# Kernel tuning notes

Hardware: AMD Instinct MI355X
Metric: run time of the kernel (lower is better)

Reference implementation:

```python
import jax, jax.numpy as jnp
import numpy as np
from jax import lax

B, S, PH, N = 4, 512, 4096, 16384
D, G, H, L, FF, GS = 1024, 128, 8, 4, 4096, 32
HD = D // H


def setup_inputs() -> dict:
    key = jax.random.key(0)
    ks = list(jax.random.split(key, 16))
    r = lambda k, sh: jax.random.normal(k, sh, jnp.float32) * 0.02
    return {
        'last_hidden': jax.random.normal(ks[0], (B, S, PH), jnp.float32),
        'current_pointcloud': jax.random.normal(ks[1], (B, N, 3), jnp.float32),
        'fp_w': r(ks[2], (D, PH)), 'fp_b': jnp.zeros((D,), jnp.float32),
        'sp_w': r(ks[3], (G * D, D)), 'sp_b': jnp.zeros((G * D,), jnp.float32),
        'pos_embed': r(ks[4], (1, G, D)),
        'ln1_w': jnp.ones((L, D), jnp.float32), 'ln1_b': jnp.zeros((L, D), jnp.float32),
        'in_w': r(ks[5], (L, 3 * D, D)), 'in_b': jnp.zeros((L, 3 * D), jnp.float32),
        'out_w': r(ks[6], (L, D, D)), 'out_b': jnp.zeros((L, D), jnp.float32),
        'ln2_w': jnp.ones((L, D), jnp.float32), 'ln2_b': jnp.zeros((L, D), jnp.float32),
        'mlp_w1': r(ks[7], (L, FF, D)), 'mlp_b1': jnp.zeros((L, FF), jnp.float32),
        'mlp_w2': r(ks[8], (L, D, FF)), 'mlp_b2': jnp.zeros((L, D), jnp.float32),
        'c1_w': r(ks[9], (D, D)), 'c1_b': jnp.zeros((D,), jnp.float32),
        'bn_g': jnp.ones((D,), jnp.float32), 'bn_beta': jnp.zeros((D,), jnp.float32),
        'bn_m': jnp.zeros((D,), jnp.float32), 'bn_v': jnp.ones((D,), jnp.float32),
        'c2_w': r(ks[10], (3 * GS, D)), 'c2_b': jnp.zeros((3 * GS,), jnp.float32),
    }


def _ln(x, w, b):
    m = jnp.mean(x, -1, keepdims=True)
    v = jnp.mean(jnp.square(x - m), -1, keepdims=True)
    return (x - m) * lax.rsqrt(v + 1e-5) * w + b


def _fps(xyz, num_samples):
    # iterative farthest point sampling; deterministic start index 0
    Bb, Nn, _ = xyz.shape
    dist0 = jnp.full((Bb, Nn), 1e10, xyz.dtype)
    far0 = jnp.zeros((Bb,), jnp.int32)

    def step(carry, _):
        dist, far = carry
        centroid = jnp.take_along_axis(xyz, far[:, None, None], axis=1)  # [B,1,3]
        d = jnp.sum(jnp.square(xyz - centroid), -1)                      # [B,N]
        dist = jnp.minimum(dist, d)
        return (dist, jnp.argmax(dist, -1).astype(jnp.int32)), far

    _, cents = lax.scan(step, (dist0, far0), None, length=num_samples)
    cents = cents.T  # [B, num_samples]
    return jnp.take_along_axis(xyz, cents[:, :, None], axis=1)  # [B,num_samples,3]


def reference(last_hidden, current_pointcloud, fp_w, fp_b, sp_w, sp_b, pos_embed,
              ln1_w, ln1_b, in_w, in_b, out_w, out_b, ln2_w, ln2_b,
              mlp_w1, mlp_b1, mlp_w2, mlp_b2,
              c1_w, c1_b, bn_g, bn_beta, bn_m, bn_v, c2_w, c2_b):
    bsz = last_hidden.shape[0]
    agg = jnp.mean(last_hidden @ fp_w.T + fp_b, axis=1)          # [B,D]
    x = (agg @ sp_w.T + sp_b).reshape(bsz, G, D)                 # [B,G,D]
    centers = _fps(current_pointcloud, G)                        # [B,G,3]
    scale = 1.0 / np.sqrt(HD).astype(np.float32)

    def block(x, p):
        l1w, l1b, iw, ib, ow, ob, l2w, l2b, w1, b1, w2, b2 = p
        xn = _ln(x + pos_embed, l1w, l1b)
        qkv = xn @ iw.T + ib                                     # [B,G,3D]
        q, k, v = jnp.split(qkv, 3, axis=-1)
        hsp = lambda t: t.reshape(bsz, G, H, HD).transpose(0, 2, 1, 3)
        q, k, v = hsp(q), hsp(k), hsp(v)
        a = jax.nn.softmax(jnp.einsum('bhqd,bhkd->bhqk', q, k) * scale, axis=-1)
        o = jnp.einsum('bhqk,bhkd->bhqd', a, v).transpose(0, 2, 1, 3).reshape(bsz, G, D)
        x = x + o @ ow.T + ob
        h = jax.nn.gelu(_ln(x, l2w, l2b) @ w1.T + b1, approximate=False)
        return x + h @ w2.T + b2, None

    x, _ = lax.scan(block, x, (ln1_w, ln1_b, in_w, in_b, out_w, out_b,
                               ln2_w, ln2_b, mlp_w1, mlp_b1, mlp_w2, mlp_b2))

    # future_predictor: 1x1 conv == per-token linear; BN in eval mode
    h = x @ c1_w.T + c1_b
    h = jax.nn.relu((h - bn_m) * lax.rsqrt(bn_v + 1e-5) * bn_g + bn_beta)
    deltas = (h @ c2_w.T + c2_b).reshape(bsz * G, GS, 3)
    pred = deltas + centers.reshape(bsz * G, 1, 3)
    return pred.reshape(bsz, G * GS, 3)
```

## Files before the change

kernel.cpp:

```cpp
#include <hip/hip_runtime.h>
#include <hip/hip_bf16.h>
#include <math.h>


typedef __bf16 bf16x8_t __attribute__((ext_vector_type(8)));
typedef float  f32x4_t  __attribute__((ext_vector_type(4)));

__device__ __forceinline__ float wredsum(float v){
#pragma unroll
  for (int o = 32; o; o >>= 1) v += __shfl_down(v, o, 64);
  return v;
}

__device__ __forceinline__ bf16x8_t pack8(float4 a, float4 b){
  bf16x8_t v;
  v[0]=(__bf16)a.x; v[1]=(__bf16)a.y; v[2]=(__bf16)a.z; v[3]=(__bf16)a.w;
  v[4]=(__bf16)b.x; v[5]=(__bf16)b.y; v[6]=(__bf16)b.z; v[7]=(__bf16)b.w;
  return v;
}

__device__ __forceinline__ void gload16(const void* g, void* l){
  __builtin_amdgcn_global_load_lds((const __attribute__((address_space(1))) unsigned int*)g,
                                   (__attribute__((address_space(3))) unsigned int*)l, 16, 0, 0);
}

__global__ __launch_bounds__(1024) void fused_front(
  const float* __restrict__ pc, float* __restrict__ centers,
  const float* __restrict__ agg, const float* __restrict__ spw,
  const float* __restrict__ spb, float* __restrict__ x,
  const float* __restrict__ inw, const float* __restrict__ outw,
  const float* __restrict__ w1, const float* __restrict__ w2,
  __bf16* __restrict__ wbf)
{
  const int bid = blockIdx.x;
  const int tid = threadIdx.x;
  if (bid < 4){
    const int b = bid;
    const int lane = tid & 63;
    const float* base = pc + (size_t)b * 16384 * 3;
    float px[16], py[16], pz[16], dist[16];
    {
      union { float4 v4[12]; float f[48]; } u;
      const float4* src = (const float4*)(base + tid * 48);
#pragma unroll
      for (int q = 0; q < 12; ++q) u.v4[q] = src[q];
#pragma unroll
      for (int j = 0; j < 16; ++j){
        px[j] = u.f[j*3]; py[j] = u.f[j*3+1]; pz[j] = u.f[j*3+2];
        dist[j] = 1e10f;
      }
    }
    __shared__ unsigned long long keyslot[128];
    for (int i = tid; i < 128; i += 1024) keyslot[i] = 0ULL;
    __syncthreads();
    float cx = base[0], cy = base[1], cz = base[2];
    for (int t = 0; t < 128; ++t){
      if (tid == 0){
        centers[(b*128+t)*3+0] = cx;
        centers[(b*128+t)*3+1] = cy;
        centers[(b*128+t)*3+2] = cz;
      }
      if (t == 127) break;
      float bmax = -1.0f; int bidx = 0;
#pragma unroll
      for (int j = 0; j < 16; ++j){
        float dx = __fsub_rn(px[j], cx);
        float dy = __fsub_rn(py[j], cy);
        float dz = __fsub_rn(pz[j], cz);
        float d  = __fadd_rn(__fadd_rn(__fmul_rn(dx,dx), __fmul_rn(dy,dy)), __fmul_rn(dz,dz));
        float nd = fminf(dist[j], d);
        dist[j] = nd;
        if (nd > bmax){ bmax = nd; bidx = tid*16 + j; }
      }
      unsigned long long key = ((unsigned long long)__float_as_uint(bmax) << 32)
                             | (unsigned long long)(0xFFFFFFFFu - (unsigned)bidx);
#pragma unroll
      for (int o = 32; o; o >>= 1){
        unsigned long long ok = __shfl_down(key, o, 64);
        if (ok > key) key = ok;
      }
      if (lane == 0) atomicMax(&keyslot[t], key);
      __syncthreads();
      const unsigned long long gk = keyslot[t];
      const unsigned gidx = 0xFFFFFFFFu - (unsigned)(gk & 0xFFFFFFFFu);
      const float* cp = base + (size_t)gidx*3;
      cx = cp[0]; cy = cp[1]; cz = cp[2];
    }
  } else if (bid < 1028){
    __shared__ float ag[4096];
    for (int i = tid; i < 4096; i += 1024) ag[i] = agg[i];
    __syncthreads();
    const int wv = tid >> 6, lane = tid & 63;
    const int rbase = ((bid - 4)*16 + wv)*8;
    for (int rr = 0; rr < 8; ++rr){
      const int row = rbase + rr;
      const float* wp = spw + (size_t)row*1024 + lane*4;
      const float4 w0 = *(const float4*)(wp      );
      const float4 wq1 = *(const float4*)(wp + 256);
      const float4 wq2 = *(const float4*)(wp + 512);
      const float4 wq3 = *(const float4*)(wp + 768);
      float acc[4];
#pragma unroll
      for (int bb = 0; bb < 4; ++bb){
        const float* gp = &ag[bb*1024 + lane*4];
        const float4 g0 = *(const float4*)(gp      );
        const float4 g1 = *(const float4*)(gp + 256);
        const float4 g2 = *(const float4*)(gp + 512);
        const float4 g3 = *(const float4*)(gp + 768);
        acc[bb] = w0.x*g0.x + w0.y*g0.y + w0.z*g0.z + w0.w*g0.w
                + wq1.x*g1.x + wq1.y*g1.y + wq1.z*g1.z + wq1.w*g1.w
                + wq2.x*g2.x + wq2.y*g2.y + wq2.z*g2.z + wq2.w*g2.w
                + wq3.x*g3.x + wq3.y*g3.y + wq3.z*g3.z + wq3.w*g3.w;
      }
      float a0 = wredsum(acc[0]);
      float a1 = wredsum(acc[1]);
      float a2 = wredsum(acc[2]);
      float a3 = wredsum(acc[3]);
      if (lane == 0){
        const float bias = spb[row];
        x[(size_t)0*131072 + row] = a0 + bias;
        x[(size_t)1*131072 + row] = a1 + bias;
        x[(size_t)2*131072 + row] = a2 + bias;
        x[(size_t)3*131072 + row] = a3 + bias;
      }
    }
  } else {
    const size_t t = (size_t)(bid - 1028)*1024 + tid;
    const size_t i = t*8;
    const float* src;
    if (i < 3145728)       src = inw  + i;
    else if (i < 4194304)  src = outw + (i-3145728);
    else if (i < 8388608)  src = w1   + (i-4194304);
    else                   src = w2   + (i-8388608);
    float4 a = *(const float4*)src, bq = *(const float4*)(src+4);
    *(bf16x8_t*)(wbf + i) = pack8(a, bq);
  }
}

__global__ __launch_bounds__(256) void partial_kernel(const float* __restrict__ lh,
                                                      float* __restrict__ part){
  const int ph = blockIdx.x*256 + threadIdx.x;
  const int sc = blockIdx.y, b = blockIdx.z;
  const float* p = lh + ((size_t)b*512 + sc*64)*4096 + ph;
  float s0=0,s1=0,s2=0,s3=0;
  for (int j = 0; j < 64; j += 4){
    s0 += p[(size_t)(j+0)*4096];
    s1 += p[(size_t)(j+1)*4096];
    s2 += p[(size_t)(j+2)*4096];
    s3 += p[(size_t)(j+3)*4096];
  }
  part[(size_t)(b*8+sc)*4096 + ph] = (s0+s1)+(s2+s3);
}

__global__ __launch_bounds__(256) void combine_kernel(const float* __restrict__ part,
                                                      float* __restrict__ mlh){
  const int i = blockIdx.x*256 + threadIdx.x;
  const int b = i >> 12, ph = i & 4095;
  float s = 0;
#pragma unroll
  for (int sc = 0; sc < 8; ++sc) s += part[(size_t)(b*8+sc)*4096 + ph];
  mlh[i] = s * (1.0f/512.0f);
}

__global__ __launch_bounds__(256) void agg_kernel(const float* __restrict__ mlh,
                                                  const float* __restrict__ fpw,
                                                  const float* __restrict__ fpb,
                                                  float* __restrict__ agg){
  const int o = blockIdx.x*4 + (threadIdx.x>>6);
  const int lane = threadIdx.x & 63;
  const int b = o >> 10, d = o & 1023;
  const float* mp = mlh + b*4096;
  const float* wp = fpw + (size_t)d*4096;
  float s = 0;
#pragma unroll 4
  for (int j = 0; j < 64; ++j){
    int ph = lane + j*64;
    s += mp[ph] * wp[ph];
  }
  s = wredsum(s);
  if (lane == 0) agg[o] = s + fpb[d];
}

__global__ __launch_bounds__(256) void ln_kernel(const float* __restrict__ x,
                                                 const float* __restrict__ pos,
                                                 const float* __restrict__ w,
                                                 const float* __restrict__ bb,
                                                 __bf16* __restrict__ out){
  const int tok = blockIdx.x, g = tok & 127, t = threadIdx.x;
  const int lane = t & 63, wv = t >> 6;
  const float* xr = x + (size_t)tok*1024;
  float v[4];
#pragma unroll
  for (int j = 0; j < 4; ++j){
    int d = t + j*256;
    float val = xr[d];
    if (pos) val += pos[g*1024 + d];
    v[j] = val;
  }
  __shared__ float r1[4], r2[4];
  float s = wredsum(v[0]+v[1]+v[2]+v[3]);
  if (lane == 0) r1[wv] = s;
  __syncthreads();
  const float mean = (r1[0]+r1[1]+r1[2]+r1[3]) * (1.0f/1024.0f);
  float sq = 0;
#pragma unroll
  for (int j = 0; j < 4; ++j){ float d0 = v[j]-mean; sq += d0*d0; }
  sq = wredsum(sq);
  if (lane == 0) r2[wv] = sq;
  __syncthreads();
  const float var = (r2[0]+r2[1]+r2[2]+r2[3]) * (1.0f/1024.0f);
  const float rs = rsqrtf(var + 1e-5f);
#pragma unroll
  for (int j = 0; j < 4; ++j){
    int d = t + j*256;
    out[(size_t)tok*1024 + d] = (__bf16)((v[j]-mean)*rs*w[d] + bb[d]);
  }
}

__global__ __launch_bounds__(256) void gemm_sk(
  const __bf16* __restrict__ A, const __bf16* __restrict__ W,
  float* __restrict__ parts, int M, int N, int K, int kc)
{
  __shared__ __bf16 As[128*64];
  __shared__ __bf16 Ws[128*64];
  const int n0 = blockIdx.x*128, m0 = blockIdx.y*128, z = blockIdx.z;
  const int tid = threadIdx.x;
  const int lane = tid & 63, w = tid >> 6;
  const int wm = w >> 1, wn = w & 1;
  const int lr = lane & 15, g = lane >> 4;
  const int kbeg = z*kc;
  const int c0 = tid, c1 = tid+256, c2 = tid+512, c3 = tid+768;
  const int r0 = c0>>3, r1 = c1>>3, r2 = c2>>3, r3 = c3>>3;
  const int s0 = ((c0&7) ^ (r0&7))*8, s1 = ((c1&7) ^ (r1&7))*8;
  const int s2 = ((c2&7) ^ (r2&7))*8, s3 = ((c3&7) ^ (r3&7))*8;
  const __bf16* pa0 = A + (size_t)(m0+r0)*K + kbeg + s0;
  const __bf16* pa1 = A + (size_t)(m0+r1)*K + kbeg + s1;
  const __bf16* pa2 = A + (size_t)(m0+r2)*K + kbeg + s2;
  const __bf16* pa3 = A + (size_t)(m0+r3)*K + kbeg + s3;
  const __bf16* pw0 = W + (size_t)(n0+r0)*K + kbeg + s0;
  const __bf16* pw1 = W + (size_t)(n0+r1)*K + kbeg + s1;
  const __bf16* pw2 = W + (size_t)(n0+r2)*K + kbeg + s2;
  const __bf16* pw3 = W + (size_t)(n0+r3)*K + kbeg + s3;
  f32x4_t acc[4][4] = {};
  for (int k0 = 0; k0 < kc; k0 += 64){
    __syncthreads();
    gload16(pa0 + k0, &As[c0*8]);
    gload16(pa1 + k0, &As[c1*8]);
    gload16(pa2 + k0, &As[c2*8]);
    gload16(pa3 + k0, &As[c3*8]);
    gload16(pw0 + k0, &Ws[c0*8]);
    gload16(pw1 + k0, &Ws[c1*8]);
    gload16(pw2 + k0, &Ws[c2*8]);
    gload16(pw3 + k0, &Ws[c3*8]);
    __syncthreads();
#pragma unroll
    for (int ks2 = 0; ks2 < 2; ++ks2){
      bf16x8_t af[4], bf[4];
#pragma unroll
      for (int f = 0; f < 4; ++f){
        const int ra = wm*64 + f*16 + lr;
        const int rb = wn*64 + f*16 + lr;
        const int lq = ks2*4 + g;
        af[f] = *(bf16x8_t*)&As[ra*64 + (lq ^ (ra&7))*8];
        bf[f] = *(bf16x8_t*)&Ws[rb*64 + (lq ^ (rb&7))*8];
      }
#pragma unroll
      for (int i = 0; i < 4; ++i)
#pragma unroll
        for (int j = 0; j < 4; ++j)
          acc[i][j] = __builtin_amdgcn_mfma_f32_16x16x32_bf16(af[i], bf[j], acc[i][j], 0, 0, 0);
    }
  }
  float* C = parts + (size_t)z*M*N;
#pragma unroll
  for (int i = 0; i < 4; ++i)
#pragma unroll
    for (int j = 0; j < 4; ++j)
#pragma unroll
      for (int r = 0; r < 4; ++r){
        const int row = m0 + wm*64 + i*16 + g*4 + r;
        const int col = n0 + wn*64 + j*16 + lr;
        C[(size_t)row*N + col] = acc[i][j][r];
      }
}

__global__ __launch_bounds__(256) void comb_qkv(const float* __restrict__ parts,
                                                const float* __restrict__ bias,
                                                __bf16* __restrict__ out){
  const int i = blockIdx.x*256 + threadIdx.x;
  const int col = i % 3072;
  out[i] = (__bf16)(parts[i] + parts[1572864 + i] + bias[col]);
}

__global__ __launch_bounds__(256) void comb_gelu(const float* __restrict__ parts,
                                                 const float* __restrict__ bias,
                                                 __bf16* __restrict__ out){
  const int i = blockIdx.x*256 + threadIdx.x;
  const int col = i & 4095;
  float v = parts[i] + parts[2097152 + i] + bias[col];
  v = v * 0.5f * (1.0f + erff(v * 0.70710678118654752440f));
  out[i] = (__bf16)v;
}

template<int MODE>
__global__ __launch_bounds__(256) void comb_res_ln(const float* __restrict__ parts, int nsplit,
                                                   const float* __restrict__ bias,
                                                   const float* __restrict__ pos,
                                                   const float* __restrict__ lw,
                                                   const float* __restrict__ lb,
                                                   float* __restrict__ x,
                                                   __bf16* __restrict__ xn){
  const int tok = blockIdx.x, gi = tok & 127, t = threadIdx.x;
  const int lane = t & 63, wv = t >> 6;
  float v[4];
#pragma unroll
  for (int j = 0; j < 4; ++j){
    const int d = t + j*256;
    const size_t idx = (size_t)tok*1024 + d;
    float s = 0;
    for (int z = 0; z < nsplit; ++z) s += parts[(size_t)z*524288 + idx];
    float val = x[idx] + s + bias[d];
    x[idx] = val;
    v[j] = val;
  }
  if (MODE == 2){
#pragma unroll
    for (int j = 0; j < 4; ++j){
      const int d = t + j*256;
      xn[(size_t)tok*1024 + d] = (__bf16)v[j];
    }
    return;
  }
  float u[4];
#pragma unroll
  for (int j = 0; j < 4; ++j){
    const int d = t + j*256;
    u[j] = v[j] + (MODE == 1 ? pos[gi*1024 + d] : 0.0f);
  }
  __shared__ float r1[4], r2[4];
  float s1 = wredsum(u[0]+u[1]+u[2]+u[3]);
  if (lane == 0) r1[wv] = s1;
  __syncthreads();
  const float mean = (r1[0]+r1[1]+r1[2]+r1[3]) * (1.0f/1024.0f);
  float sq = 0;
#pragma unroll
  for (int j = 0; j < 4; ++j){ float d0 = u[j]-mean; sq += d0*d0; }
  sq = wredsum(sq);
  if (lane == 0) r2[wv] = sq;
  __syncthreads();
  const float var = (r2[0]+r2[1]+r2[2]+r2[3]) * (1.0f/1024.0f);
  const float rs = rsqrtf(var + 1e-5f);
#pragma unroll
  for (int j = 0; j < 4; ++j){
    const int d = t + j*256;
    xn[(size_t)tok*1024 + d] = (__bf16)((u[j]-mean)*rs*lw[d] + lb[d]);
  }
}

__global__ __launch_bounds__(256) void attn_fused(const __bf16* __restrict__ qkv,
                                                  __bf16* __restrict__ O,
                                                  const float* __restrict__ cs0,
                                                  const float* __restrict__ cs1,
                                                  const float* __restrict__ cs2,
                                                  const float* __restrict__ cs3,
                                                  __bf16* __restrict__ cdst,
                                                  int nch){
  if (blockIdx.x >= 64){
    const int t = (blockIdx.x - 64)*256 + threadIdx.x;
    if (t < nch){
      const size_t i = (size_t)t*8;
      const float* src;
      if (cs1 == nullptr){
        src = cs0 + i;
      } else {
        if (i < 3145728)       src = cs0 + i;
        else if (i < 4194304)  src = cs1 + (i-3145728);
        else if (i < 8388608)  src = cs2 + (i-4194304);
        else                   src = cs3 + (i-8388608);
      }
      float4 a = *(const float4*)src, bq = *(const float4*)(src+4);
      *(bf16x8_t*)(cdst + i) = pack8(a, bq);
    }
    return;
  }
  const int bh = blockIdx.x >> 1, half = blockIdx.x & 1;
  const int b = bh>>3, h = bh&7;
  const int tid = threadIdx.x, w = tid>>6, lane = tid&63;
  const int lr = lane&15, g = lane>>4;
  __shared__ __bf16 vt[128*128];
  __shared__ __bf16 pl[4*2048];
  {
    const int n = tid >> 1, kh = tid & 1;
    const __bf16* vbase = qkv + (size_t)(b*128)*3072 + 2048 + h*128 + n;
#pragma unroll
    for (int jb = 0; jb < 8; ++jb){
      bf16x8_t pk;
#pragma unroll
      for (int e = 0; e < 8; ++e) pk[e] = vbase[(size_t)(kh*64 + jb*8 + e)*3072];
      const int cb = kh*8 + jb;
      *(bf16x8_t*)&vt[n*128 + ((cb ^ (n&7)) * 8)] = pk;
    }
  }
  const __bf16* qbase = qkv + (size_t)(b*128)*3072 + h*128;
  const __bf16* kbase = qbase + 1024;
  const int qrow0 = half*64 + w*16;
  f32x4_t acc[8] = {};
#pragma unroll
  for (int ks = 0; ks < 4; ++ks){
    bf16x8_t aq, bk[8];
    aq = *(const bf16x8_t*)(qbase + (size_t)(qrow0 + lr)*3072 + ks*32 + g*8);
#pragma unroll
    for (int j = 0; j < 8; ++j)
      bk[j] = *(const bf16x8_t*)(kbase + (size_t)(j*16 + lr)*3072 + ks*32 + g*8);
#pragma unroll
    for (int j = 0; j < 8; ++j)
      acc[j] = __builtin_amdgcn_mfma_f32_16x16x32_bf16(aq, bk[j], acc[j], 0, 0, 0);
  }
  __syncthreads();
  const float scale = 0.088388347648318447f;
#pragma unroll
  for (int r = 0; r < 4; ++r){
    const int row = g*4 + r;
    float sv[8];
    float mx = -1e30f;
#pragma unroll
    for (int j = 0; j < 8; ++j){ sv[j] = acc[j][r]*scale; mx = fmaxf(mx, sv[j]); }
#pragma unroll
    for (int o = 1; o < 16; o <<= 1) mx = fmaxf(mx, __shfl_xor(mx, o, 64));
    float s = 0;
#pragma unroll
    for (int j = 0; j < 8; ++j){ sv[j] = expf(sv[j]-mx); s += sv[j]; }
#pragma unroll
    for (int o = 1; o < 16; o <<= 1) s += __shfl_xor(s, o, 64);
    const float inv = 1.0f/s;
#pragma unroll
    for (int j = 0; j < 8; ++j){
      const int col = j*16 + lr;
      const int slot = (col>>3) ^ (row&7);
      pl[w*2048 + row*128 + slot*8 + (lr&7)] = (__bf16)(sv[j]*inv);
    }
  }
  __syncthreads();
  f32x4_t acc2[8] = {};
#pragma unroll
  for (int ks = 0; ks < 4; ++ks){
    bf16x8_t ap, bv[8];
    {
      const int row = lr;
      const int slot = (ks*4 + g) ^ (row&7);
      ap = *(bf16x8_t*)&pl[w*2048 + row*128 + slot*8];
    }
#pragma unroll
    for (int j = 0; j < 8; ++j){
      const int rowv = j*16 + lr;
      const int cb = ks*4 + g;
      bv[j] = *(bf16x8_t*)&vt[rowv*128 + ((cb ^ (rowv&7))*8)];
    }
#pragma unroll
    for (int j = 0; j < 8; ++j)
      acc2[j] = __builtin_amdgcn_mfma_f32_16x16x32_bf16(ap, bv[j], acc2[j], 0, 0, 0);
  }
#pragma unroll
  for (int j = 0; j < 8; ++j)
#pragma unroll
    for (int r = 0; r < 4; ++r){
      const int row = qrow0 + g*4 + r;
      const int col = j*16 + lr;
      O[(size_t)(b*128+row)*1024 + h*128 + col] = (__bf16)acc2[j][r];
    }
}

__global__ __launch_bounds__(256) void head_kernel(const float* __restrict__ parts,
                                                   const float* __restrict__ c1b,
                                                   const float* __restrict__ bnm,
                                                   const float* __restrict__ bnv,
                                                   const float* __restrict__ bng,
                                                   const float* __restrict__ bnb,
                                                   const float* __restrict__ c2w,
                                                   const float* __restrict__ c2b,
                                                   const float* __restrict__ centers,
                                                   float* __restrict__ out){
  const int tok = blockIdx.x, t = threadIdx.x;
  const int wv = t >> 6, lane = t & 63;
  __shared__ float hrow[1024];
#pragma unroll
  for (int j = 0; j < 4; ++j){
    const int d = t + j*256;
    const size_t idx = (size_t)tok*1024 + d;
    float s = 0;
#pragma unroll
    for (int z = 0; z < 8; ++z) s += parts[(size_t)z*524288 + idx];
    float v = s + c1b[d];
    v = (v - bnm[d]) * rsqrtf(bnv[d] + 1e-5f) * bng[d] + bnb[d];
    hrow[d] = fmaxf(v, 0.0f);
  }
  __syncthreads();
  for (int i = 0; i < 24; ++i){
    const int n = wv*24 + i;
    const float* wp = c2w + (size_t)n*1024;
    float s = 0;
#pragma unroll 4
    for (int j = 0; j < 16; ++j){
      const int k = lane + j*64;
      s += hrow[k] * wp[k];
    }
    s = wredsum(s);
    if (lane == 0) out[(size_t)tok*96 + n] = s + c2b[n] + centers[tok*3 + (n % 3)];
  }
}

extern "C" void kernel_launch(void* const* d_in, const int* in_sizes, int n_in,
                              void* d_out, int out_size, void* d_ws, size_t ws_size,
                              hipStream_t stream){
  const float* lh   = (const float*)d_in[0];
  const float* pc   = (const float*)d_in[1];
  const float* fpw  = (const float*)d_in[2];
  const float* fpb  = (const float*)d_in[3];
  const float* spw  = (const float*)d_in[4];
  const float* spb  = (const float*)d_in[5];
  const float* pos  = (const float*)d_in[6];
  const float* ln1w = (const float*)d_in[7];
  const float* ln1b = (const float*)d_in[8];
  const float* inw  = (const float*)d_in[9];
  const float* inb  = (const float*)d_in[10];
  const float* outw = (const float*)d_in[11];
  const float* outb = (const float*)d_in[12];
  const float* ln2w = (const float*)d_in[13];
  const float* ln2b = (const float*)d_in[14];
  const float* w1   = (const float*)d_in[15];
  const float* b1   = (const float*)d_in[16];
  const float* w2   = (const float*)d_in[17];
  const float* b2   = (const float*)d_in[18];
  const float* c1w  = (const float*)d_in[19];
  const float* c1b  = (const float*)d_in[20];
  const float* bng  = (const float*)d_in[21];
  const float* bnbt = (const float*)d_in[22];
  const float* bnm  = (const float*)d_in[23];
  const float* bnv  = (const float*)d_in[24];
  const float* c2w  = (const float*)d_in[25];
  const float* c2b  = (const float*)d_in[26];
  float* out = (float*)d_out;

  float* f = (float*)d_ws;
  float* parts = f;              f += 16*524288;
  float* part  = f;              f += 131072;
  float* mlh   = f;              f += 16384;
  float* agg   = f;              f += 4096;
  float* x     = f;              f += 524288;
  float* cent  = f;              f += 2048;
  __bf16* bfp = (__bf16*)f;
  __bf16* xn   = bfp;            bfp += 524288;
  __bf16* qkv  = bfp;            bfp += 1572864;
  __bf16* obuf = bfp;            bfp += 524288;
  __bf16* hbf  = bfp;            bfp += 2097152;
  __bf16* xbf  = bfp;            bfp += 524288;
  __bf16* wbf  = bfp;            bfp += 51380224;

  partial_kernel<<<dim3(16,8,4), 256, 0, stream>>>(lh, part);
  combine_kernel<<<64, 256, 0, stream>>>(part, mlh);
  agg_kernel<<<1024, 256, 0, stream>>>(mlh, fpw, fpb, agg);
  fused_front<<<2564, 1024, 0, stream>>>(pc, cent, agg, spw, spb, x,
                                         inw, outw, w1, w2, wbf);
  ln_kernel<<<512, 256, 0, stream>>>(x, pos, ln1w, ln1b, xn);

  for (int l = 0; l < 4; ++l){
    const __bf16* wl = wbf + (size_t)l*12582912;
    gemm_sk<<<dim3(24,4,2), 256, 0, stream>>>(xn, wl, parts, 512, 3072, 1024, 512);
    comb_qkv<<<6144, 256, 0, stream>>>(parts, inb + l*3072, qkv);
    if (l < 3)
      attn_fused<<<64 + 6144, 256, 0, stream>>>(qkv, obuf,
          inw + (size_t)(l+1)*3145728, outw + (size_t)(l+1)*1048576,
          w1 + (size_t)(l+1)*4194304, w2 + (size_t)(l+1)*4194304,
          wbf + (size_t)(l+1)*12582912, 1572864);
    else
      attn_fused<<<64 + 512, 256, 0, stream>>>(qkv, obuf,
          c1w, nullptr, nullptr, nullptr, wbf + 50331648, 131072);
    gemm_sk<<<dim3(8,4,8), 256, 0, stream>>>(obuf, wl + 3145728, parts, 512, 1024, 1024, 128);
    comb_res_ln<0><<<512, 256, 0, stream>>>(parts, 8, outb + l*1024, nullptr,
                                            ln2w + l*1024, ln2b + l*1024, x, xn);
    gemm_sk<<<dim3(32,4,2), 256, 0, stream>>>(xn, wl + 4194304, parts, 512, 4096, 1024, 512);
    comb_gelu<<<8192, 256, 0, stream>>>(parts, b1 + l*4096, hbf);
    gemm_sk<<<dim3(8,4,8), 256, 0, stream>>>(hbf, wl + 8388608, parts, 512, 1024, 4096, 512);
    if (l < 3)
      comb_res_ln<1><<<512, 256, 0, stream>>>(parts, 8, b2 + l*1024, pos,
                                              ln1w + (l+1)*1024, ln1b + (l+1)*1024, x, xn);
    else
      comb_res_ln<2><<<512, 256, 0, stream>>>(parts, 8, b2 + l*1024, nullptr,
                                              nullptr, nullptr, x, xbf);
  }

  gemm_sk<<<dim3(8,4,8), 256, 0, stream>>>(xbf, wbf + 50331648, parts, 512, 1024, 1024, 128);
  head_kernel<<<512, 256, 0, stream>>>(parts, c1b, bnm, bnv, bng, bnbt, c2w, c2b, cent, out);
}
```

Measured before the change: 794.1 us.

## Fuse bias and GELU epilogues into non-split-K GEMMs for QKV and MLP1

Replaces the split-K GEMM plus separate combine kernels for the QKV projection and the first MLP layer with a new 64x128-tile GEMM that covers the full K dimension and applies bias (and exact GELU) in its epilogue, writing bf16 directly. This removes the fp32 partial-sum round trip through global memory and two kernel launches per layer. In exchange each block runs the whole K loop with a single-buffered LDS stage and no split-K parallelism, though the smaller M tile keeps the grid at 192 or 256 blocks.

```diff
diff --git a/kernel.cpp b/kernel.cpp
--- a/kernel.cpp
+++ b/kernel.cpp
@@ -284,22 +284,76 @@
       }
 }
 
-__global__ __launch_bounds__(256) void comb_qkv(const float* __restrict__ parts,
-                                                const float* __restrict__ bias,
-                                                __bf16* __restrict__ out){
-  const int i = blockIdx.x*256 + threadIdx.x;
-  const int col = i % 3072;
-  out[i] = (__bf16)(parts[i] + parts[1572864 + i] + bias[col]);
-}
-
-__global__ __launch_bounds__(256) void comb_gelu(const float* __restrict__ parts,
-                                                 const float* __restrict__ bias,
-                                                 __bf16* __restrict__ out){
-  const int i = blockIdx.x*256 + threadIdx.x;
-  const int col = i & 4095;
-  float v = parts[i] + parts[2097152 + i] + bias[col];
-  v = v * 0.5f * (1.0f + erff(v * 0.70710678118654752440f));
-  out[i] = (__bf16)v;
+template<int EPI>
+__global__ __launch_bounds__(256) void gemm64f(
+  const __bf16* __restrict__ A, const __bf16* __restrict__ W,
+  const float* __restrict__ bias, __bf16* __restrict__ C,
+  int M, int N, int K)
+{
+  __shared__ __bf16 As[64*64];
+  __shared__ __bf16 Ws[128*64];
+  const int n0 = blockIdx.x*128, m0 = blockIdx.y*64;
+  const int tid = threadIdx.x;
+  const int lane = tid & 63, w = tid >> 6;
+  const int wm = w >> 1, wn = w & 1;
+  const int lr = lane & 15, g = lane >> 4;
+  const int cA0 = tid, cA1 = tid+256;
+  const int rA0 = cA0>>3, rA1 = cA1>>3;
+  const int sA0 = ((cA0&7)^(rA0&7))*8, sA1 = ((cA1&7)^(rA1&7))*8;
+  const int cW0 = tid, cW1 = tid+256, cW2 = tid+512, cW3 = tid+768;
+  const int rW0 = cW0>>3, rW1 = cW1>>3, rW2 = cW2>>3, rW3 = cW3>>3;
+  const int sW0 = ((cW0&7)^(rW0&7))*8, sW1 = ((cW1&7)^(rW1&7))*8;
+  const int sW2 = ((cW2&7)^(rW2&7))*8, sW3 = ((cW3&7)^(rW3&7))*8;
+  const __bf16* pa0 = A + (size_t)(m0+rA0)*K + sA0;
+  const __bf16* pa1 = A + (size_t)(m0+rA1)*K + sA1;
+  const __bf16* pw0 = W + (size_t)(n0+rW0)*K + sW0;
+  const __bf16* pw1 = W + (size_t)(n0+rW1)*K + sW1;
+  const __bf16* pw2 = W + (size_t)(n0+rW2)*K + sW2;
+  const __bf16* pw3 = W + (size_t)(n0+rW3)*K + sW3;
+  f32x4_t acc[2][4] = {};
+  for (int k0 = 0; k0 < K; k0 += 64){
+    __syncthreads();
+    gload16(pa0 + k0, &As[cA0*8]);
+    gload16(pa1 + k0, &As[cA1*8]);
+    gload16(pw0 + k0, &Ws[cW0*8]);
+    gload16(pw1 + k0, &Ws[cW1*8]);
+    gload16(pw2 + k0, &Ws[cW2*8]);
+    gload16(pw3 + k0, &Ws[cW3*8]);
+    __syncthreads();
+#pragma unroll
+    for (int ks2 = 0; ks2 < 2; ++ks2){
+      bf16x8_t af[2], bf[4];
+#pragma unroll
+      for (int i = 0; i < 2; ++i){
+        const int ra = wm*32 + i*16 + lr;
+        const int lq = ks2*4 + g;
+        af[i] = *(bf16x8_t*)&As[ra*64 + (lq ^ (ra&7))*8];
+      }
+#pragma unroll
+      for (int j = 0; j < 4; ++j){
+        const int rb = wn*64 + j*16 + lr;
+        const int lq = ks2*4 + g;
+        bf[j] = *(bf16x8_t*)&Ws[rb*64 + (lq ^ (rb&7))*8];
+      }
+#pragma unroll
+      for (int i = 0; i < 2; ++i)
+#pragma unroll
+        for (int j = 0; j < 4; ++j)
+          acc[i][j] = __builtin_amdgcn_mfma_f32_16x16x32_bf16(af[i], bf[j], acc[i][j], 0, 0, 0);
+    }
+  }
+#pragma unroll
+  for (int i = 0; i < 2; ++i)
+#pragma unroll
+    for (int j = 0; j < 4; ++j)
+#pragma unroll
+      for (int r = 0; r < 4; ++r){
+        const int row = m0 + wm*32 + i*16 + g*4 + r;
+        const int col = n0 + wn*64 + j*16 + lr;
+        float v = acc[i][j][r] + bias[col];
+        if (EPI == 2) v = v * 0.5f * (1.0f + erff(v * 0.70710678118654752440f));
+        C[(size_t)row*N + col] = (__bf16)v;
+      }
 }
 
 template<int MODE>
@@ -565,8 +619,7 @@
 
   for (int l = 0; l < 4; ++l){
     const __bf16* wl = wbf + (size_t)l*12582912;
-    gemm_sk<<<dim3(24,4,2), 256, 0, stream>>>(xn, wl, parts, 512, 3072, 1024, 512);
-    comb_qkv<<<6144, 256, 0, stream>>>(parts, inb + l*3072, qkv);
+    gemm64f<0><<<dim3(24,8), 256, 0, stream>>>(xn, wl, inb + l*3072, qkv, 512, 3072, 1024);
     if (l < 3)
       attn_fused<<<64 + 6144, 256, 0, stream>>>(qkv, obuf,
           inw + (size_t)(l+1)*3145728, outw + (size_t)(l+1)*1048576,
@@ -578,8 +631,7 @@
     gemm_sk<<<dim3(8,4,8), 256, 0, stream>>>(obuf, wl + 3145728, parts, 512, 1024, 1024, 128);
     comb_res_ln<0><<<512, 256, 0, stream>>>(parts, 8, outb + l*1024, nullptr,
                                             ln2w + l*1024, ln2b + l*1024, x, xn);
-    gemm_sk<<<dim3(32,4,2), 256, 0, stream>>>(xn, wl + 4194304, parts, 512, 4096, 1024, 512);
-    comb_gelu<<<8192, 256, 0, stream>>>(parts, b1 + l*4096, hbf);
+    gemm64f<2><<<dim3(32,8), 256, 0, stream>>>(xn, wl + 4194304, b1 + l*4096, hbf, 512, 4096, 1024);
     gemm_sk<<<dim3(8,4,8), 256, 0, stream>>>(hbf, wl + 8388608, parts, 512, 1024, 4096, 512);
     if (l < 3)
       comb_res_ln<1><<<512, 256, 0, stream>>>(parts, 8, b2 + l*1024, pos,
```

Result: faster. 756.8 us (-4.7%).
